# Kernel optimization log

Measured on AMD Instinct MI355X. Metric: run time of the kernel, lower is better.

The kernel has to match this reference:

```python
import jax, jax.numpy as jnp
import numpy as np

# Static hyperparameters matching init_kwargs
G, N, D = 8, 8, 8          # groups, filters/group, kernel depth (c = G*D, o = G*N)
W, KS = 16, 4              # kernel width (time window), time stride
AH, AS = 2, 2              # activate_height, activate_stride (freq box-sum window)
C, F = 64, 128             # input channels, embedding (freq bins)
O = G * N                  # out_channels


def setup_inputs() -> dict:
    key = jax.random.key(0)
    kx, kw = jax.random.split(key)
    x = jax.random.normal(kx, (16, C, F, 256), dtype=jnp.float32)
    # xavier-uniform for weight (o, d, e, w)
    fan_in = D * F * W
    fan_out = fan_in  # torch xavier on 4D: fan computed over receptive field; bound below matches scale
    bound = float(np.sqrt(6.0 / (fan_in + fan_out)))
    weight = jax.random.uniform(kw, (O, D, F, W), dtype=jnp.float32, minval=-bound, maxval=bound)
    return {"x": x, "weight": weight}


def reference(x, weight):
    b, c, f, T = x.shape
    t = (T - W) // KS + 1
    # unfold time: x[..., ti*KS + wi] -> [b, c, f, t, W]
    idx = jnp.arange(t)[:, None] * KS + jnp.arange(W)[None, :]
    xu = x[..., idx]
    # split channels (g d) row-major, matching einops 'b (g d) f t w'
    xg = xu.reshape(b, G, D, f, t, W)
    wg = weight.reshape(G, N, D, f, W)
    # fused: multiply-broadcast then sum over d and w (the ones-kernel conv sums
    # over depth d and full width w); height window handled below.
    z = jnp.einsum('bgdftw,gndfw->btgnf', xg, wg)  # [b, t, G, N, f]
    z = z.reshape(b, t, O, f)
    # box-sum over freq with window AH, stride AS ('valid')
    fp = (f - AH) // AS + 1
    pidx = jnp.arange(fp)[:, None] * AS + jnp.arange(AH)
    y = z[..., pidx].sum(-1)  # [b, t, O, fp]
    return jnp.transpose(y, (0, 2, 3, 1))  # [b, O, fp, t]
```

## Files before the change

### kernel.cpp

```cpp
#include <hip/hip_runtime.h>


namespace {
constexpr int kB  = 16;
constexpr int kC  = 64;
constexpr int kF  = 128;
constexpr int kT  = 256;
constexpr int kG  = 8;
constexpr int kD  = 8;
constexpr int kN  = 8;
constexpr int kW  = 16;
constexpr int kKS = 4;
constexpr int kNT = 61;
constexpr int kO  = 64;
constexpr int kFP = 64;
constexpr int kWStride = kD * kF * kW;
}

__global__ __launch_bounds__(256, 2)
void lc2d_kernel(const float* __restrict__ x,
                 const float* __restrict__ wt,
                 float* __restrict__ out) {
  const int lane = threadIdx.x & 63;
  const int wq   = threadIdx.x >> 6;
  const int fi   = blockIdx.x;
  const int g    = blockIdx.y;

  const int tc   = (lane < kNT - 1) ? lane : (kNT - 1);
  const int tau0 = tc * kKS;

  const float* xb[4];
#pragma unroll
  for (int bb = 0; bb < 4; ++bb) {
    const int b = wq * 4 + bb;
    xb[bb] = x + (((size_t)b * kC + g * kD) * kF + fi * 2) * kT + tau0;
  }
  const float* wbase = wt + ((size_t)(g * kN) * kD * kF + fi * 2) * (size_t)kW;

  float acc[4][kN];
#pragma unroll
  for (int bb = 0; bb < 4; ++bb)
#pragma unroll
    for (int n = 0; n < kN; ++n) acc[bb][n] = 0.f;

  float4 cur[4][4];
#pragma unroll
  for (int bb = 0; bb < 4; ++bb)
#pragma unroll
    for (int q = 0; q < 4; ++q) cur[bb][q] = ((const float4*)xb[bb])[q];

#pragma unroll 2
  for (int it = 0; it < 16; ++it) {
    const int nx = (it < 15) ? it + 1 : 15;
    const size_t roff = ((size_t)(nx >> 1) * kF + (nx & 1)) * kT;
    float4 pre[4][4];
#pragma unroll
    for (int bb = 0; bb < 4; ++bb) {
      const float* xr = xb[bb] + roff;
#pragma unroll
      for (int q = 0; q < 4; ++q) pre[bb][q] = ((const float4*)xr)[q];
    }

    const float* wr0 = wbase + (((size_t)(it >> 1) * kF + (it & 1))) * kW;
#pragma unroll
    for (int n = 0; n < kN; ++n) {
      const float* wr = wr0 + (size_t)n * kWStride;
      const float4 w0 = ((const float4*)wr)[0];
      const float4 w1 = ((const float4*)wr)[1];
      const float4 w2 = ((const float4*)wr)[2];
      const float4 w3 = ((const float4*)wr)[3];
#pragma unroll
      for (int bb = 0; bb < 4; ++bb) {
        float a = acc[bb][n];
        a = fmaf(cur[bb][0].x, w0.x, a);
        a = fmaf(cur[bb][0].y, w0.y, a);
        a = fmaf(cur[bb][0].z, w0.z, a);
        a = fmaf(cur[bb][0].w, w0.w, a);
        a = fmaf(cur[bb][1].x, w1.x, a);
        a = fmaf(cur[bb][1].y, w1.y, a);
        a = fmaf(cur[bb][1].z, w1.z, a);
        a = fmaf(cur[bb][1].w, w1.w, a);
        a = fmaf(cur[bb][2].x, w2.x, a);
        a = fmaf(cur[bb][2].y, w2.y, a);
        a = fmaf(cur[bb][2].z, w2.z, a);
        a = fmaf(cur[bb][2].w, w2.w, a);
        a = fmaf(cur[bb][3].x, w3.x, a);
        a = fmaf(cur[bb][3].y, w3.y, a);
        a = fmaf(cur[bb][3].z, w3.z, a);
        a = fmaf(cur[bb][3].w, w3.w, a);
        acc[bb][n] = a;
      }
    }

#pragma unroll
    for (int bb = 0; bb < 4; ++bb)
#pragma unroll
      for (int q = 0; q < 4; ++q) cur[bb][q] = pre[bb][q];
  }

  if (lane < kNT) {
    const size_t s = (size_t)kFP * kNT;
#pragma unroll
    for (int bb = 0; bb < 4; ++bb) {
      const int b = wq * 4 + bb;
      float* ob = out + (((size_t)b * kO + g * kN) * kFP + fi) * (size_t)kNT + lane;
#pragma unroll
      for (int n = 0; n < kN; ++n) ob[(size_t)n * s] = acc[bb][n];
    }
  }
}

extern "C" void kernel_launch(void* const* d_in, const int* in_sizes, int n_in,
                              void* d_out, int out_size, void* d_ws, size_t ws_size,
                              hipStream_t stream) {
  const float* x  = (const float*)d_in[0];
  const float* wt = (const float*)d_in[1];
  float* out      = (float*)d_out;

  dim3 grid(kFP, kG, 1);
  lc2d_kernel<<<grid, 256, 0, stream>>>(x, wt, out);
}
```

Baseline: 207.9 us.

## Split batch across grid z so each wave handles one batch element

Each block previously had every wave compute four batch elements with register double-buffered x rows. Now the grid adds a z dimension over batch groups, so each wave computes one batch element, the register prefetch is dropped, and launch bounds are raised to allow more resident waves. The aim is more parallelism and occupancy to hide load latency. In exchange, each loaded weight is reused across fewer batch elements, so weight load traffic per FMA grows fourfold.

Measured after the change: 214.8 us. 3.3% more time.

```diff
diff --git a/kernel.cpp b/kernel.cpp
--- a/kernel.cpp
+++ b/kernel.cpp
@@ -2,11 +2,9 @@
 
 
 namespace {
-constexpr int kB  = 16;
 constexpr int kC  = 64;
 constexpr int kF  = 128;
 constexpr int kT  = 256;
-constexpr int kG  = 8;
 constexpr int kD  = 8;
 constexpr int kN  = 8;
 constexpr int kW  = 16;
@@ -14,99 +12,86 @@
 constexpr int kNT = 61;
 constexpr int kO  = 64;
 constexpr int kFP = 64;
-constexpr int kWStride = kD * kF * kW;
+constexpr int kQN = 4096;
+constexpr int kQD = 512;
+constexpr int kQF = 4;
 }
 
-__global__ __launch_bounds__(256, 2)
+__global__ __launch_bounds__(256, 8)
 void lc2d_kernel(const float* __restrict__ x,
                  const float* __restrict__ wt,
                  float* __restrict__ out) {
   const int lane = threadIdx.x & 63;
-  const int wq   = threadIdx.x >> 6;
+  const int wv   = threadIdx.x >> 6;
   const int fi   = blockIdx.x;
   const int g    = blockIdx.y;
+  const int b    = blockIdx.z * 4 + wv;
 
-  const int tc   = (lane < kNT - 1) ? lane : (kNT - 1);
+  const int tc   = (lane < kNT) ? lane : (kNT - 1);
   const int tau0 = tc * kKS;
 
-  const float* xb[4];
+  const float* xb =
+      x + (((size_t)b * kC + g * kD) * kF + fi * 2) * kT + tau0;
+  const float4* wb =
+      (const float4*)(wt + ((size_t)(g * kN) * kD * kF + (size_t)fi * 2) * kW);
+
+  float acc[kN];
 #pragma unroll
-  for (int bb = 0; bb < 4; ++bb) {
-    const int b = wq * 4 + bb;
-    xb[bb] = x + (((size_t)b * kC + g * kD) * kF + fi * 2) * kT + tau0;
-  }
-  const float* wbase = wt + ((size_t)(g * kN) * kD * kF + fi * 2) * (size_t)kW;
-
-  float acc[4][kN];
-#pragma unroll
-  for (int bb = 0; bb < 4; ++bb)
-#pragma unroll
-    for (int n = 0; n < kN; ++n) acc[bb][n] = 0.f;
-
-  float4 cur[4][4];
-#pragma unroll
-  for (int bb = 0; bb < 4; ++bb)
-#pragma unroll
-    for (int q = 0; q < 4; ++q) cur[bb][q] = ((const float4*)xb[bb])[q];
+  for (int n = 0; n < kN; ++n) acc[n] = 0.f;
 
 #pragma unroll 2
   for (int it = 0; it < 16; ++it) {
-    const int nx = (it < 15) ? it + 1 : 15;
-    const size_t roff = ((size_t)(nx >> 1) * kF + (nx & 1)) * kT;
-    float4 pre[4][4];
+    const int d  = it >> 1;
+    const int fr = it & 1;
+
+    const float* xr = xb + ((size_t)d * kF + fr) * kT;
+    const float4 c0 = ((const float4*)xr)[0];
+    const float4 c1 = ((const float4*)xr)[1];
+    const float4 c2 = ((const float4*)xr)[2];
+    const float4 c3 = ((const float4*)xr)[3];
+
+    const float4* wit = wb + d * kQD + fr * kQF;
+
 #pragma unroll
-    for (int bb = 0; bb < 4; ++bb) {
-      const float* xr = xb[bb] + roff;
+    for (int nb = 0; nb < 2; ++nb) {
+      float4 w[16];
 #pragma unroll
-      for (int q = 0; q < 4; ++q) pre[bb][q] = ((const float4*)xr)[q];
-    }
-
-    const float* wr0 = wbase + (((size_t)(it >> 1) * kF + (it & 1))) * kW;
+      for (int j = 0; j < 16; ++j)
+        w[j] = wit[(size_t)(nb * 4 + (j >> 2)) * kQN + (j & 3)];
 #pragma unroll
-    for (int n = 0; n < kN; ++n) {
-      const float* wr = wr0 + (size_t)n * kWStride;
-      const float4 w0 = ((const float4*)wr)[0];
-      const float4 w1 = ((const float4*)wr)[1];
-      const float4 w2 = ((const float4*)wr)[2];
-      const float4 w3 = ((const float4*)wr)[3];
-#pragma unroll
-      for (int bb = 0; bb < 4; ++bb) {
-        float a = acc[bb][n];
-        a = fmaf(cur[bb][0].x, w0.x, a);
-        a = fmaf(cur[bb][0].y, w0.y, a);
-        a = fmaf(cur[bb][0].z, w0.z, a);
-        a = fmaf(cur[bb][0].w, w0.w, a);
-        a = fmaf(cur[bb][1].x, w1.x, a);
-        a = fmaf(cur[bb][1].y, w1.y, a);
-        a = fmaf(cur[bb][1].z, w1.z, a);
-        a = fmaf(cur[bb][1].w, w1.w, a);
-        a = fmaf(cur[bb][2].x, w2.x, a);
-        a = fmaf(cur[bb][2].y, w2.y, a);
-        a = fmaf(cur[bb][2].z, w2.z, a);
-        a = fmaf(cur[bb][2].w, w2.w, a);
-        a = fmaf(cur[bb][3].x, w3.x, a);
-        a = fmaf(cur[bb][3].y, w3.y, a);
-        a = fmaf(cur[bb][3].z, w3.z, a);
-        a = fmaf(cur[bb][3].w, w3.w, a);
-        acc[bb][n] = a;
+      for (int nn = 0; nn < 4; ++nn) {
+        const float4 w0 = w[nn * 4 + 0];
+        const float4 w1 = w[nn * 4 + 1];
+        const float4 w2 = w[nn * 4 + 2];
+        const float4 w3 = w[nn * 4 + 3];
+        float a = acc[nb * 4 + nn];
+        a = fmaf(c0.x, w0.x, a);
+        a = fmaf(c0.y, w0.y, a);
+        a = fmaf(c0.z, w0.z, a);
+        a = fmaf(c0.w, w0.w, a);
+        a = fmaf(c1.x, w1.x, a);
+        a = fmaf(c1.y, w1.y, a);
+        a = fmaf(c1.z, w1.z, a);
+        a = fmaf(c1.w, w1.w, a);
+        a = fmaf(c2.x, w2.x, a);
+        a = fmaf(c2.y, w2.y, a);
+        a = fmaf(c2.z, w2.z, a);
+        a = fmaf(c2.w, w2.w, a);
+        a = fmaf(c3.x, w3.x, a);
+        a = fmaf(c3.y, w3.y, a);
+        a = fmaf(c3.z, w3.z, a);
+        a = fmaf(c3.w, w3.w, a);
+        acc[nb * 4 + nn] = a;
       }
     }
-
-#pragma unroll
-    for (int bb = 0; bb < 4; ++bb)
-#pragma unroll
-      for (int q = 0; q < 4; ++q) cur[bb][q] = pre[bb][q];
   }
 
   if (lane < kNT) {
     const size_t s = (size_t)kFP * kNT;
+    float* ob =
+        out + (((size_t)b * kO + g * kN) * kFP + fi) * (size_t)kNT + lane;
 #pragma unroll
-    for (int bb = 0; bb < 4; ++bb) {
-      const int b = wq * 4 + bb;
-      float* ob = out + (((size_t)b * kO + g * kN) * kFP + fi) * (size_t)kNT + lane;
-#pragma unroll
-      for (int n = 0; n < kN; ++n) ob[(size_t)n * s] = acc[bb][n];
-    }
+    for (int n = 0; n < kN; ++n) ob[(size_t)n * s] = acc[n];
   }
 }
 
@@ -117,6 +102,6 @@
   const float* wt = (const float*)d_in[1];
   float* out      = (float*)d_out;
 
-  dim3 grid(kFP, kG, 1);
+  dim3 grid(kFP, 8, 4);
   lc2d_kernel<<<grid, 256, 0, stream>>>(x, wt, out);
 }
```
